# Performance work log

Measured on AMD Instinct MI355X. Metric: run time of the kernel, lower is better.

Reference implementation:

```python
import jax, jax.numpy as jnp
import numpy as np

NUM_KNOTS = 10
DEGREE = 3
NUM_BASIS = NUM_KNOTS + DEGREE - 1  # 12
IN_FEATURES = 512
OUT_FEATURES = 512


def _interval_bounds():
    # t = linspace(0,1,num_knots); segment i covers [t[max(0,i-deg+1)], t[min(i+1,K-1)])
    t = np.linspace(0.0, 1.0, NUM_KNOTS, dtype=np.float32)
    idx = np.arange(NUM_BASIS)
    lower = t[np.maximum(0, idx - (DEGREE - 1))]
    upper = t[np.minimum(idx + 1, NUM_KNOTS - 1)]
    return jnp.asarray(lower), jnp.asarray(upper)


def setup_inputs() -> dict:
    key = jax.random.key(0)
    kx, kc = jax.random.split(key)
    x = jax.random.uniform(kx, (8, 2048, IN_FEATURES), dtype=jnp.float32)
    # coeffs for spline (i=out, j=in): torch indexes splines[i*in_features+j]
    coeffs = jax.random.normal(kc, (OUT_FEATURES, IN_FEATURES, NUM_BASIS), dtype=jnp.float32)
    return {"x": x, "coeffs": coeffs}


def reference(x, coeffs):
    lower, upper = _interval_bounds()  # [NUM_BASIS] each
    # piecewise-constant basis masks: [b, s, in, NUM_BASIS]
    xe = x[..., None]
    basis = ((xe >= lower) & (xe < upper)).astype(x.dtype)
    # out[b,s,i] = sum_j sum_k basis[b,s,j,k] * coeffs[i,j,k]
    return jnp.einsum("bsjk,ijk->bsi", basis, coeffs)
```

## Files before the change

kernel.cpp:

```cpp
#include <hip/hip_runtime.h>

#define MTOT 16384
#define NFEAT 512
#define KTOT 4608

typedef float f32x4 __attribute__((ext_vector_type(4)));
typedef short s16x8 __attribute__((ext_vector_type(8)));

__device__ __forceinline__ int div9(int c) { return (c * 7282) >> 16; }

#define GLDS(GP, LP) __builtin_amdgcn_global_load_lds( \
    (const __attribute__((address_space(1))) void*)(GP), \
    (__attribute__((address_space(3))) void*)(LP), 16, 0, 0)

__device__ __forceinline__ s16x8 decode_frag(unsigned code) {
  unsigned nb0 = code & 15u, nb1 = code >> 4;
  unsigned p0 = nb0 - 1u, p1 = nb1 - 1u;
  unsigned long long v0 = (nb0 ? 0x3F80ull : 0ull) << ((p0 & 3u) << 4);
  unsigned long long v1 = (nb1 ? 0x3F80ull : 0ull) << ((p1 & 3u) << 4);
  unsigned long long lo = (p0 < 4u ? v0 : 0ull) | (p1 < 4u ? v1 : 0ull);
  unsigned long long hi = (p0 < 4u ? 0ull : v0) | (p1 < 4u ? 0ull : v1);
  union { unsigned long long q[2]; s16x8 v; } u;
  u.q[0] = lo; u.q[1] = hi;
  return u.v;
}

__global__ __launch_bounds__(256) void prep(const float* __restrict__ x,
                                            const float* __restrict__ coeffs,
                                            unsigned char* __restrict__ codeT,
                                            unsigned short* __restrict__ Bmat) {
  __shared__ unsigned char segt[64][68];
  const int bx = blockIdx.x;
  const int tid = threadIdx.x;
  if (bx < 2048) {
    const int i = bx >> 2, q = bx & 3;
    const float* cb = coeffs + (size_t)i * 6144;
#pragma unroll
    for (int p = 0; p < 5; ++p) {
      int kl = p * 256 + tid;
      if (kl < 1152) {
        int k = q * 1152 + kl;
        int j = div9(k), s = k - j * 9;
        float v = cb[j * 12 + s] + cb[j * 12 + s + 1] + cb[j * 12 + s + 2];
        unsigned u = __float_as_uint(v);
        unsigned rn = (u + 0x7FFFu + ((u >> 16) & 1u)) >> 16;
        Bmat[(size_t)i * KTOT + k] = (unsigned short)rn;
      }
    }
  } else {
    const int bb = bx - 2048;
    const int mt = bb >> 3;
    const int jt = bb & 7;
    const int m0 = mt * 64;
    const float4* x4 = (const float4*)x;
    const float T1 = (float)(1.0/9.0), T2 = (float)(2.0/9.0), T3 = (float)(3.0/9.0),
                T4 = (float)(4.0/9.0), T5 = (float)(5.0/9.0), T6 = (float)(6.0/9.0),
                T7 = (float)(7.0/9.0), T8 = (float)(8.0/9.0);
#pragma unroll
    for (int it = 0; it < 4; ++it) {
      int f = it * 256 + tid;
      int m = f >> 4, jq = f & 15;
      float4 v = x4[(size_t)(m0 + m) * 128 + jt * 16 + jq];
      uchar4 sv;
      { float xv = v.x; sv.x = (unsigned char)((xv>=T1)+(xv>=T2)+(xv>=T3)+(xv>=T4)+(xv>=T5)+(xv>=T6)+(xv>=T7)+(xv>=T8)); }
      { float xv = v.y; sv.y = (unsigned char)((xv>=T1)+(xv>=T2)+(xv>=T3)+(xv>=T4)+(xv>=T5)+(xv>=T6)+(xv>=T7)+(xv>=T8)); }
      { float xv = v.z; sv.z = (unsigned char)((xv>=T1)+(xv>=T2)+(xv>=T3)+(xv>=T4)+(xv>=T5)+(xv>=T6)+(xv>=T7)+(xv>=T8)); }
      { float xv = v.w; sv.w = (unsigned char)((xv>=T1)+(xv>=T2)+(xv>=T3)+(xv>=T4)+(xv>=T5)+(xv>=T6)+(xv>=T7)+(xv>=T8)); }
      *(uchar4*)&segt[m][jq * 4] = sv;
    }
    __syncthreads();
#pragma unroll
    for (int p = 0; p < 5; ++p) {
      int u = p * 256 + tid;
      if (u < 1152) {
        int gl = u >> 4, mq = u & 15;
        int c0 = jt * 576 + gl * 8;
        int j0 = div9(c0), j1 = div9(c0 + 7);
        int j0l = j0 - jt * 64, j1l = j1 - jt * 64;
        uchar4 ob;
        unsigned char* pb = (unsigned char*)&ob;
#pragma unroll
        for (int c = 0; c < 4; ++c) {
          int m = mq * 4 + c;
          int s0 = segt[m][j0l];
          int pos0 = j0 * 9 + s0 - c0;
          unsigned code = (pos0 >= 0 && pos0 < 8) ? (unsigned)(pos0 + 1) : 0u;
          if (j1 != j0) {
            int s1 = segt[m][j1l];
            int pos1 = j1 * 9 + s1 - c0;
            if (pos1 < 8) code |= (unsigned)(pos1 + 1) << 4;
          }
          pb[c] = (unsigned char)code;
        }
        *(uchar4*)(codeT + (size_t)(jt * 72 + gl) * MTOT + m0 + mq * 4) = ob;
      }
    }
  }
}

__global__ __launch_bounds__(256, 2) void kan_gemm(const unsigned char* __restrict__ codeT,
                                                   const unsigned short* __restrict__ Bmat,
                                                   float* __restrict__ out) {
  __shared__ __align__(16) short Blds[4][16 * 512];
  const int tid = threadIdx.x;
  const int lane = tid & 63;
  const int wid = tid >> 6;
  const int lm = lane & 15;
  const int lq = lane >> 4;
  const int bx = blockIdx.x;
  const int rr8 = bx & 7, qq = bx >> 3;
  const int nt = rr8 & 3;
  const int mt = qq * 2 + (rr8 >> 2);
  const int m0 = mt * 128, n0 = nt * 128;
  const int wr = wid;

  const unsigned short* gB0 = Bmat + (size_t)(n0 + (wid * 2 + 0) * 16 + lm) * KTOT + lq * 8;
  const unsigned short* gB1 = Bmat + (size_t)(n0 + (wid * 2 + 1) * 16 + lm) * KTOT + lq * 8;
  const unsigned char* gC0 = codeT + (size_t)lq * MTOT + m0 + wr * 32 + lm;
  const unsigned char* gC1 = codeT + (size_t)(4 + lq) * MTOT + m0 + wr * 32 + lm;

  f32x4 acc[2][8] = {};
  s16x8 afX[4], afY[4];
  unsigned char crQ[4][4];

#define CRLOAD(SET) do { \
    crQ[SET][0] = gC0[0]; crQ[SET][1] = gC1[0]; \
    crQ[SET][2] = gC0[16]; crQ[SET][3] = gC1[16]; \
    gC0 += (size_t)8 * MTOT; gC1 += (size_t)8 * MTOT; } while (0)

#define ISSUE_B(SLOT) do { \
    short* base = &Blds[SLOT][0] + wid * 2048; \
    GLDS(gB0,      base);        \
    GLDS(gB0 + 32, base + 512);  \
    GLDS(gB1,      base + 1024); \
    GLDS(gB1 + 32, base + 1536); \
    gB0 += 64; gB1 += 64; } while (0)

#define DECODE(SET, AF) do { \
    _Pragma("unroll") \
    for (int f = 0; f < 4; ++f) AF[f] = decode_frag(crQ[SET][f]); } while (0)

#define COMPUTE(AF, SLOT) do { \
    __builtin_amdgcn_s_setprio(1); \
    _Pragma("unroll") \
    for (int ks = 0; ks < 2; ++ks) { \
      s16x8 bf[8]; \
      _Pragma("unroll") \
      for (int ns = 0; ns < 8; ++ns) \
        bf[ns] = *(const s16x8*)&Blds[SLOT][(ns * 2 + ks) * 512 + lane * 8]; \
      _Pragma("unroll") \
      for (int ms = 0; ms < 2; ++ms) \
        _Pragma("unroll") \
        for (int ns = 0; ns < 8; ++ns) \
          acc[ms][ns] = __builtin_amdgcn_mfma_f32_16x16x32_bf16(AF[ms * 2 + ks], bf[ns], acc[ms][ns], 0, 0, 0); \
    } \
    __builtin_amdgcn_s_setprio(0); } while (0)

#define VWAIT(N) asm volatile("s_waitcnt vmcnt(" #N ")" ::: "memory")
#define FENCE()  asm volatile("" ::: "memory")
#define BAR()    __builtin_amdgcn_s_barrier()

  CRLOAD(0); FENCE();
  CRLOAD(1); ISSUE_B(0); FENCE();
  CRLOAD(2); ISSUE_B(1); FENCE();
  CRLOAD(3); ISSUE_B(2); FENCE();
  VWAIT(24);
  DECODE(0, afX);

#pragma unroll 1
  for (int k = 0; k < 17; ++k) {
    VWAIT(16); BAR();
    CRLOAD(0); ISSUE_B(3);
    DECODE(1, afY);
    COMPUTE(afX, 0);

    VWAIT(16); BAR();
    CRLOAD(1); ISSUE_B(0);
    DECODE(2, afX);
    COMPUTE(afY, 1);

    VWAIT(16); BAR();
    CRLOAD(2); ISSUE_B(1);
    DECODE(3, afY);
    COMPUTE(afX, 2);

    VWAIT(16); BAR();
    CRLOAD(3); ISSUE_B(2);
    DECODE(0, afX);
    COMPUTE(afY, 3);
  }

  VWAIT(16); BAR();
  ISSUE_B(3);
  DECODE(1, afY);
  COMPUTE(afX, 0);

  VWAIT(12); BAR();
  DECODE(2, afX);
  COMPUTE(afY, 1);

  VWAIT(4); BAR();
  DECODE(3, afY);
  COMPUTE(afX, 2);

  VWAIT(0); BAR();
  COMPUTE(afY, 3);

#pragma unroll
  for (int ms = 0; ms < 2; ++ms) {
#pragma unroll
    for (int ns = 0; ns < 8; ++ns) {
      int tok = m0 + wr * 32 + ms * 16 + lq * 4;
      int col = n0 + ns * 16 + lm;
      float* op = out + (size_t)tok * NFEAT + col;
#pragma unroll
      for (int rg = 0; rg < 4; ++rg) op[(size_t)rg * NFEAT] = acc[ms][ns][rg];
    }
  }
#undef CRLOAD
#undef ISSUE_B
#undef DECODE
#undef COMPUTE
#undef VWAIT
#undef FENCE
#undef BAR
}

extern "C" void kernel_launch(void* const* d_in, const int* in_sizes, int n_in,
                              void* d_out, int out_size, void* d_ws, size_t ws_size,
                              hipStream_t stream) {
  const float* x = (const float*)d_in[0];
  const float* coeffs = (const float*)d_in[1];
  float* out = (float*)d_out;
  unsigned char* codeT = (unsigned char*)d_ws;
  unsigned short* Bmat = (unsigned short*)((char*)d_ws + (size_t)576 * MTOT);

  prep<<<dim3(4096), dim3(256), 0, stream>>>(x, coeffs, codeT, Bmat);
  kan_gemm<<<dim3(512), dim3(256), 0, stream>>>(codeT, Bmat, out);
}
```

Measured before the change: 177.9 us.

## Use two waves per block with 64x128 per-wave tiles and packed code loads

Cuts the GEMM block from four waves to two, each computing a 64-row by 128-column tile with 32 accumulator fragments, which doubles A-fragment reuse per LDS B read. The prep kernel now interleaves its code bytes so each lane can fetch four rows' codes with one 32-bit load instead of separate byte loads. Wait counts are retuned for the new load counts. The cost is far higher register pressure at one block per launch-bound slot and fewer waves to hide latency.

```diff
diff --git a/kernel.cpp b/kernel.cpp
--- a/kernel.cpp
+++ b/kernel.cpp
@@ -81,7 +81,7 @@
         unsigned char* pb = (unsigned char*)&ob;
 #pragma unroll
         for (int c = 0; c < 4; ++c) {
-          int m = mq * 4 + c;
+          int m = mq + c * 16;
           int s0 = segt[m][j0l];
           int pos0 = j0 * 9 + s0 - c0;
           unsigned code = (pos0 >= 0 && pos0 < 8) ? (unsigned)(pos0 + 1) : 0u;
@@ -98,7 +98,7 @@
   }
 }
 
-__global__ __launch_bounds__(256, 2) void kan_gemm(const unsigned char* __restrict__ codeT,
+__global__ __launch_bounds__(128, 1) void kan_gemm(const unsigned char* __restrict__ codeT,
                                                    const unsigned short* __restrict__ Bmat,
                                                    float* __restrict__ out) {
   __shared__ __align__(16) short Blds[4][16 * 512];
@@ -112,33 +112,36 @@
   const int nt = rr8 & 3;
   const int mt = qq * 2 + (rr8 >> 2);
   const int m0 = mt * 128, n0 = nt * 128;
-  const int wr = wid;
-
-  const unsigned short* gB0 = Bmat + (size_t)(n0 + (wid * 2 + 0) * 16 + lm) * KTOT + lq * 8;
-  const unsigned short* gB1 = Bmat + (size_t)(n0 + (wid * 2 + 1) * 16 + lm) * KTOT + lq * 8;
-  const unsigned char* gC0 = codeT + (size_t)lq * MTOT + m0 + wr * 32 + lm;
-  const unsigned char* gC1 = codeT + (size_t)(4 + lq) * MTOT + m0 + wr * 32 + lm;
-
-  f32x4 acc[2][8] = {};
-  s16x8 afX[4], afY[4];
-  unsigned char crQ[4][4];
+
+  const unsigned short* gB0 = Bmat + (size_t)(n0 + (wid * 4 + 0) * 16 + lm) * KTOT + lq * 8;
+  const unsigned short* gB1 = Bmat + (size_t)(n0 + (wid * 4 + 1) * 16 + lm) * KTOT + lq * 8;
+  const unsigned short* gB2 = Bmat + (size_t)(n0 + (wid * 4 + 2) * 16 + lm) * KTOT + lq * 8;
+  const unsigned short* gB3 = Bmat + (size_t)(n0 + (wid * 4 + 3) * 16 + lm) * KTOT + lq * 8;
+  const unsigned* gC0 = (const unsigned*)(codeT + (size_t)lq * MTOT + m0 + wid * 64) + lm;
+  const unsigned* gC1 = (const unsigned*)(codeT + (size_t)(4 + lq) * MTOT + m0 + wid * 64) + lm;
+
+  f32x4 acc[4][8] = {};
+  s16x8 afX[8], afY[8];
+  unsigned crQ[4][2];
 
 #define CRLOAD(SET) do { \
     crQ[SET][0] = gC0[0]; crQ[SET][1] = gC1[0]; \
-    crQ[SET][2] = gC0[16]; crQ[SET][3] = gC1[16]; \
-    gC0 += (size_t)8 * MTOT; gC1 += (size_t)8 * MTOT; } while (0)
+    gC0 += 2 * MTOT; gC1 += 2 * MTOT; } while (0)
 
 #define ISSUE_B(SLOT) do { \
-    short* base = &Blds[SLOT][0] + wid * 2048; \
-    GLDS(gB0,      base);        \
-    GLDS(gB0 + 32, base + 512);  \
-    GLDS(gB1,      base + 1024); \
-    GLDS(gB1 + 32, base + 1536); \
-    gB0 += 64; gB1 += 64; } while (0)
+    short* base = &Blds[SLOT][0] + wid * 4096; \
+    GLDS(gB0, base);        GLDS(gB0 + 32, base + 512);  \
+    GLDS(gB1, base + 1024); GLDS(gB1 + 32, base + 1536); \
+    GLDS(gB2, base + 2048); GLDS(gB2 + 32, base + 2560); \
+    GLDS(gB3, base + 3072); GLDS(gB3 + 32, base + 3584); \
+    gB0 += 64; gB1 += 64; gB2 += 64; gB3 += 64; } while (0)
 
 #define DECODE(SET, AF) do { \
     _Pragma("unroll") \
-    for (int f = 0; f < 4; ++f) AF[f] = decode_frag(crQ[SET][f]); } while (0)
+    for (int c = 0; c < 4; ++c) { \
+      AF[c * 2 + 0] = decode_frag((crQ[SET][0] >> (c * 8)) & 255u); \
+      AF[c * 2 + 1] = decode_frag((crQ[SET][1] >> (c * 8)) & 255u); \
+    } } while (0)
 
 #define COMPUTE(AF, SLOT) do { \
     __builtin_amdgcn_s_setprio(1); \
@@ -149,7 +152,7 @@
       for (int ns = 0; ns < 8; ++ns) \
         bf[ns] = *(const s16x8*)&Blds[SLOT][(ns * 2 + ks) * 512 + lane * 8]; \
       _Pragma("unroll") \
-      for (int ms = 0; ms < 2; ++ms) \
+      for (int ms = 0; ms < 4; ++ms) \
         _Pragma("unroll") \
         for (int ns = 0; ns < 8; ++ns) \
           acc[ms][ns] = __builtin_amdgcn_mfma_f32_16x16x32_bf16(AF[ms * 2 + ks], bf[ns], acc[ms][ns], 0, 0, 0); \
@@ -164,42 +167,42 @@
   CRLOAD(1); ISSUE_B(0); FENCE();
   CRLOAD(2); ISSUE_B(1); FENCE();
   CRLOAD(3); ISSUE_B(2); FENCE();
-  VWAIT(24);
+  VWAIT(30);
   DECODE(0, afX);
 
 #pragma unroll 1
   for (int k = 0; k < 17; ++k) {
-    VWAIT(16); BAR();
+    VWAIT(20); BAR();
     CRLOAD(0); ISSUE_B(3);
     DECODE(1, afY);
     COMPUTE(afX, 0);
 
-    VWAIT(16); BAR();
+    VWAIT(20); BAR();
     CRLOAD(1); ISSUE_B(0);
     DECODE(2, afX);
     COMPUTE(afY, 1);
 
-    VWAIT(16); BAR();
+    VWAIT(20); BAR();
     CRLOAD(2); ISSUE_B(1);
     DECODE(3, afY);
     COMPUTE(afX, 2);
 
-    VWAIT(16); BAR();
+    VWAIT(20); BAR();
     CRLOAD(3); ISSUE_B(2);
     DECODE(0, afX);
     COMPUTE(afY, 3);
   }
 
-  VWAIT(16); BAR();
+  VWAIT(20); BAR();
   ISSUE_B(3);
   DECODE(1, afY);
   COMPUTE(afX, 0);
 
-  VWAIT(12); BAR();
+  VWAIT(18); BAR();
   DECODE(2, afX);
   COMPUTE(afY, 1);
 
-  VWAIT(4); BAR();
+  VWAIT(8); BAR();
   DECODE(3, afY);
   COMPUTE(afX, 2);
 
@@ -207,10 +210,10 @@
   COMPUTE(afY, 3);
 
 #pragma unroll
-  for (int ms = 0; ms < 2; ++ms) {
+  for (int ms = 0; ms < 4; ++ms) {
 #pragma unroll
     for (int ns = 0; ns < 8; ++ns) {
-      int tok = m0 + wr * 32 + ms * 16 + lq * 4;
+      int tok = m0 + wid * 64 + ms * 16 + lq * 4;
       int col = n0 + ns * 16 + lm;
       float* op = out + (size_t)tok * NFEAT + col;
 #pragma unroll
@@ -236,5 +239,5 @@
   unsigned short* Bmat = (unsigned short*)((char*)d_ws + (size_t)576 * MTOT);
 
   prep<<<dim3(4096), dim3(256), 0, stream>>>(x, coeffs, codeT, Bmat);
-  kan_gemm<<<dim3(512), dim3(256), 0, stream>>>(codeT, Bmat, out);
-}
+  kan_gemm<<<dim3(512), dim3(128), 0, stream>>>(codeT, Bmat, out);
+}
```

After: 192.0 us. +7.9%, slower.
